# Optimization experiments

Measured on AMD Instinct MI355X. Metric: run time of the kernel, lower is better.

## Reference

```python
import jax, jax.numpy as jnp
import numpy as np

N_NODES = 100000
N_EDGES = 1600000
N_GRAPHS = 256
F_NODE, F_EDGE, HID, OUT = 64, 16, 128, 128
BN_SCALE = 1.0 / np.sqrt(1.0 + 1e-5)  # BatchNorm eval with running mean 0, var 1


def setup_inputs() -> dict:
    key = jax.random.key(0)
    ks = iter(jax.random.split(key, 64))
    inp = {}
    inp["x"] = jax.random.normal(next(ks), (N_NODES, F_NODE), dtype=jnp.float32)
    inp["edge_attr"] = jax.random.normal(next(ks), (N_EDGES, F_EDGE), dtype=jnp.float32)
    inp["edge_index"] = jax.random.randint(next(ks), (2, N_EDGES), 0, N_NODES)
    inp["batch"] = jnp.sort(jax.random.randint(next(ks), (N_NODES,), 0, N_GRAPHS))

    def p(shape, scale):
        return (jax.random.normal(next(ks), shape, dtype=jnp.float32) * scale)

    in_dims = [F_NODE, HID, HID]
    for i, d in enumerate(in_dims):
        inp[f"el_w{i}"] = p((F_EDGE, d), F_EDGE ** -0.5)
        inp[f"el_b{i}"] = jnp.zeros((d,), jnp.float32)
        inp[f"c{i}_w1"] = p((d, HID), d ** -0.5)
        inp[f"c{i}_b1"] = jnp.zeros((HID,), jnp.float32)
        inp[f"c{i}_g"] = jnp.ones((HID,), jnp.float32)
        inp[f"c{i}_bt"] = jnp.zeros((HID,), jnp.float32)
        inp[f"c{i}_w2"] = p((HID, HID), HID ** -0.5)
        inp[f"c{i}_b2"] = jnp.zeros((HID,), jnp.float32)
    inp["o_w1"] = p((HID, OUT), HID ** -0.5)
    inp["o_b1"] = jnp.zeros((OUT,), jnp.float32)
    inp["o_w2"] = p((OUT, OUT), OUT ** -0.5)
    inp["o_b2"] = jnp.zeros((OUT,), jnp.float32)
    return inp


def reference(x, edge_attr,
              el_w0, el_b0, c0_w1, c0_b1, c0_g, c0_bt, c0_w2, c0_b2,
              el_w1, el_b1, c1_w1, c1_b1, c1_g, c1_bt, c1_w2, c1_b2,
              el_w2, el_b2, c2_w1, c2_b1, c2_g, c2_bt, c2_w2, c2_b2,
              o_w1, o_b1, o_w2, o_b2,
              edge_index, batch):
    src, dst = edge_index[0], edge_index[1]
    n = x.shape[0]
    layers = [
        (el_w0, el_b0, c0_w1, c0_b1, c0_g, c0_bt, c0_w2, c0_b2),
        (el_w1, el_b1, c1_w1, c1_b1, c1_g, c1_bt, c1_w2, c1_b2),
        (el_w2, el_b2, c2_w1, c2_b1, c2_g, c2_bt, c2_w2, c2_b2),
    ]
    h = x
    for (ew, eb, w1, b1, g, bt, w2, b2) in layers:
        ea = edge_attr @ ew + eb                              # [E, d]
        msg = jax.nn.relu(h[src] + ea)                        # GINEConv message
        agg = jax.ops.segment_sum(msg, dst, num_segments=n)   # scatter-sum to targets
        hh = h + agg                                          # (1+eps)*x + aggr, eps=0
        hh = hh @ w1 + b1                                     # MLP: Linear
        hh = g * (hh * BN_SCALE) + bt                         # BatchNorm1d (eval)
        hh = jax.nn.relu(hh)
        hh = hh @ w2 + b2                                     # MLP: Linear
        h = jax.nn.relu(hh)                                   # dropout(p=0, eval) + act
    s = jax.ops.segment_sum(h, batch, num_segments=N_GRAPHS)
    cnt = jax.ops.segment_sum(jnp.ones((n,), h.dtype), batch, num_segments=N_GRAPHS)
    pooled = s / jnp.maximum(cnt, 1.0)[:, None]               # scatter-mean pooling
    out = jax.nn.relu(pooled @ o_w1 + o_b1) @ o_w2 + o_b2     # out_lin
    return out
```

## Files before the change

kernel.cpp:

```cpp
#include <hip/hip_runtime.h>
#include <hip/hip_fp16.h>
#include <cstdint>
#include <cstddef>

#define N_NODES_C  100000
#define N_EDGES_C  1600000
#define N_GRAPHS_C 256
#define HID_C      128
#define BN_SCALE_C 0.9999950000374997f

#define SCAN_B 1024
#define SCAN_NB ((N_NODES_C + SCAN_B - 1) / SCAN_B)

typedef _Float16 h2 __attribute__((ext_vector_type(2)));
typedef _Float16 h4 __attribute__((ext_vector_type(4)));
typedef _Float16 h8 __attribute__((ext_vector_type(8)));
typedef float    f4 __attribute__((ext_vector_type(4)));

struct __align__(16) EA8 { h2 p[4]; };
struct __align__(8)  HQ  { h2 a, b; };
struct __align__(16) H8  { __half2 v[4]; };

#if defined(__has_builtin)
#  if __has_builtin(__builtin_amdgcn_fdot2)
#    define HAVE_FDOT2 1
#  endif
#endif
#ifndef HAVE_FDOT2
#  define HAVE_FDOT2 0
#endif

__device__ __forceinline__ float fdot2_(h2 a, h2 b, float c)
{
#if HAVE_FDOT2
    return __builtin_amdgcn_fdot2(a, b, c, false);
#else
    return c + (float)a[0] * (float)b[0] + (float)a[1] * (float)b[1];
#endif
}

__global__ __launch_bounds__(256) void hist_kernel(
    const int* __restrict__ dst, int* __restrict__ counts, int n_edges)
{
    int e = blockIdx.x * 256 + threadIdx.x;
    if (e < n_edges) atomicAdd(&counts[dst[e]], 1);
}

__global__ __launch_bounds__(SCAN_B) void scan1_kernel(
    const int* __restrict__ counts, int* __restrict__ incl,
    int* __restrict__ blocksums, int n)
{
    __shared__ int sdata[SCAN_B];
    const int lid = threadIdx.x;
    const int i = blockIdx.x * SCAN_B + lid;
    sdata[lid] = (i < n) ? counts[i] : 0;
    __syncthreads();
#pragma unroll
    for (int off = 1; off < SCAN_B; off <<= 1) {
        int t = (lid >= off) ? sdata[lid - off] : 0;
        __syncthreads();
        sdata[lid] += t;
        __syncthreads();
    }
    if (i < n) incl[i] = sdata[lid];
    if (lid == SCAN_B - 1) blocksums[blockIdx.x] = sdata[lid];
}

__global__ void scan2_kernel(const int* __restrict__ blocksums,
                             int* __restrict__ blockoffs, int nb)
{
    if (threadIdx.x == 0 && blockIdx.x == 0) {
        int off = 0;
        for (int b = 0; b < nb; ++b) { blockoffs[b] = off; off += blocksums[b]; }
    }
}

__global__ __launch_bounds__(SCAN_B) void scan3_kernel(
    int* __restrict__ incl, const int* __restrict__ blockoffs, int n)
{
    const int i = blockIdx.x * SCAN_B + threadIdx.x;
    if (i < n) incl[i] += blockoffs[blockIdx.x];
}

__global__ __launch_bounds__(256) void initrows_kernel(
    const int* __restrict__ incl, const int* __restrict__ counts,
    int* __restrict__ rowstart, int* __restrict__ cursor, int n)
{
    const int i = blockIdx.x * 256 + threadIdx.x;
    if (i < n) {
        const int rs = incl[i] - counts[i];
        rowstart[i] = rs;
        cursor[i]   = rs;
    }
}

__global__ __launch_bounds__(256) void scatter_ea_kernel(
    const int* __restrict__ src, const int* __restrict__ dst,
    int* __restrict__ cursor, int* __restrict__ perm_src,
    const float* __restrict__ edge_attr, __half* __restrict__ ea_f16,
    int n_edges)
{
    const int e = blockIdx.x * 256 + threadIdx.x;
    if (e >= n_edges) return;

    const float4* p = (const float4*)(edge_attr + (size_t)e * 16);
    const float4 q0 = p[0], q1 = p[1], q2 = p[2], q3 = p[3];

    const int pos = atomicAdd(&cursor[dst[e]], 1);
    perm_src[pos] = src[e];

    H8 a, b;
    a.v[0] = __floats2half2_rn(q0.x, q0.y);
    a.v[1] = __floats2half2_rn(q0.z, q0.w);
    a.v[2] = __floats2half2_rn(q1.x, q1.y);
    a.v[3] = __floats2half2_rn(q1.z, q1.w);
    b.v[0] = __floats2half2_rn(q2.x, q2.y);
    b.v[1] = __floats2half2_rn(q2.z, q2.w);
    b.v[2] = __floats2half2_rn(q3.x, q3.y);
    b.v[3] = __floats2half2_rn(q3.z, q3.w);
    H8* o = (H8*)(ea_f16 + (size_t)pos * 16);
    o[0] = a;
    o[1] = b;
}

__global__ __launch_bounds__(256) void cast_f16_kernel(
    const float* __restrict__ in, _Float16* __restrict__ out, int n4)
{
    const int i = blockIdx.x * 256 + threadIdx.x;
    if (i >= n4) return;
    const float4 v = ((const float4*)in)[i];
    h4 o; o[0] = (_Float16)v.x; o[1] = (_Float16)v.y;
    o[2] = (_Float16)v.z; o[3] = (_Float16)v.w;
    *(h4*)(out + (size_t)i * 4) = o;
}

__global__ __launch_bounds__(256) void transpose_w_kernel(
    const float* __restrict__ w, _Float16* __restrict__ wt, int K, int N)
{
    const int i = blockIdx.x * 256 + threadIdx.x;
    if (i >= K * N) return;
    const int n = i / K;
    const int k = i - n * K;
    wt[(size_t)n * K + k] = (_Float16)w[(size_t)k * N + n];
}

__device__ __forceinline__ float4 eamlp2(const EA8 a0, const EA8 c0,
                                         const h2 (*ew2h)[4], const float4 ebv)
{
    float4 m = {ebv.x, ebv.y, ebv.z, ebv.w};
#pragma unroll
    for (int k = 0; k < 4; ++k) {
        m.x = fdot2_(a0.p[k], ew2h[k][0], m.x);
        m.y = fdot2_(a0.p[k], ew2h[k][1], m.y);
        m.z = fdot2_(a0.p[k], ew2h[k][2], m.z);
        m.w = fdot2_(a0.p[k], ew2h[k][3], m.w);
    }
#pragma unroll
    for (int k = 0; k < 4; ++k) {
        m.x = fdot2_(c0.p[k], ew2h[4 + k][0], m.x);
        m.y = fdot2_(c0.p[k], ew2h[4 + k][1], m.y);
        m.z = fdot2_(c0.p[k], ew2h[4 + k][2], m.z);
        m.w = fdot2_(c0.p[k], ew2h[4 + k][3], m.w);
    }
    return m;
}

template<int DIN>
__global__ __launch_bounds__(256) void gine_agg_kernel(
    const _Float16* __restrict__ hin, const _Float16* __restrict__ ea16,
    const int* __restrict__ perm_src,
    const int* __restrict__ rowstart, const int* __restrict__ rowend,
    const float* __restrict__ ew, const float* __restrict__ eb,
    _Float16* __restrict__ x16, int n_nodes)
{
    constexpr int NQ    = DIN / 4;
    constexpr int SLOTS = 256 / NQ;
    const int fq   = threadIdx.x & (NQ - 1);
    const int slot = threadIdx.x / NQ;
    const int v = blockIdx.x * SLOTS + slot;
    if (v >= n_nodes) return;

    h2 ew2h[8][4];
#pragma unroll
    for (int k2 = 0; k2 < 8; ++k2)
#pragma unroll
        for (int fi = 0; fi < 4; ++fi) {
            h2 t;
            t[0] = (_Float16)ew[(size_t)(2 * k2)     * DIN + fq * 4 + fi];
            t[1] = (_Float16)ew[(size_t)(2 * k2 + 1) * DIN + fq * 4 + fi];
            ew2h[k2][fi] = t;
        }
    const float4 ebv = *(const float4*)(eb + fq * 4);

    const int s0 = rowstart[v];
    const int s1 = rowend[v];

    float4 acc = {0.f, 0.f, 0.f, 0.f};
    int j = s0;

    for (; j + 4 <= s1; j += 4) {
        const int sn0 = perm_src[j + 0];
        const int sn1 = perm_src[j + 1];
        const int sn2 = perm_src[j + 2];
        const int sn3 = perm_src[j + 3];
        const EA8* pe = (const EA8*)(ea16 + (size_t)j * 16);
        const EA8 a0 = pe[0], c0 = pe[1], a1 = pe[2], c1 = pe[3];
        const EA8 a2 = pe[4], c2 = pe[5], a3 = pe[6], c3 = pe[7];
        const HQ hq0 = *(const HQ*)(hin + (size_t)sn0 * DIN + fq * 4);
        const HQ hq1 = *(const HQ*)(hin + (size_t)sn1 * DIN + fq * 4);
        const HQ hq2 = *(const HQ*)(hin + (size_t)sn2 * DIN + fq * 4);
        const HQ hq3 = *(const HQ*)(hin + (size_t)sn3 * DIN + fq * 4);

        const float4 m0 = eamlp2(a0, c0, ew2h, ebv);
        const float4 m1 = eamlp2(a1, c1, ew2h, ebv);
        const float4 m2 = eamlp2(a2, c2, ew2h, ebv);
        const float4 m3 = eamlp2(a3, c3, ew2h, ebv);

        acc.x += fmaxf(m0.x + (float)hq0.a[0], 0.f) + fmaxf(m1.x + (float)hq1.a[0], 0.f)
               + fmaxf(m2.x + (float)hq2.a[0], 0.f) + fmaxf(m3.x + (float)hq3.a[0], 0.f);
        acc.y += fmaxf(m0.y + (float)hq0.a[1], 0.f) + fmaxf(m1.y + (float)hq1.a[1], 0.f)
               + fmaxf(m2.y + (float)hq2.a[1], 0.f) + fmaxf(m3.y + (float)hq3.a[1], 0.f);
        acc.z += fmaxf(m0.z + (float)hq0.b[0], 0.f) + fmaxf(m1.z + (float)hq1.b[0], 0.f)
               + fmaxf(m2.z + (float)hq2.b[0], 0.f) + fmaxf(m3.z + (float)hq3.b[0], 0.f);
        acc.w += fmaxf(m0.w + (float)hq0.b[1], 0.f) + fmaxf(m1.w + (float)hq1.b[1], 0.f)
               + fmaxf(m2.w + (float)hq2.b[1], 0.f) + fmaxf(m3.w + (float)hq3.b[1], 0.f);
    }
    if (j + 2 <= s1) {
        const int sn0 = perm_src[j + 0];
        const int sn1 = perm_src[j + 1];
        const EA8* pe = (const EA8*)(ea16 + (size_t)j * 16);
        const EA8 a0 = pe[0], c0 = pe[1], a1 = pe[2], c1 = pe[3];
        const HQ hq0 = *(const HQ*)(hin + (size_t)sn0 * DIN + fq * 4);
        const HQ hq1 = *(const HQ*)(hin + (size_t)sn1 * DIN + fq * 4);
        const float4 m0 = eamlp2(a0, c0, ew2h, ebv);
        const float4 m1 = eamlp2(a1, c1, ew2h, ebv);
        acc.x += fmaxf(m0.x + (float)hq0.a[0], 0.f) + fmaxf(m1.x + (float)hq1.a[0], 0.f);
        acc.y += fmaxf(m0.y + (float)hq0.a[1], 0.f) + fmaxf(m1.y + (float)hq1.a[1], 0.f);
        acc.z += fmaxf(m0.z + (float)hq0.b[0], 0.f) + fmaxf(m1.z + (float)hq1.b[0], 0.f);
        acc.w += fmaxf(m0.w + (float)hq0.b[1], 0.f) + fmaxf(m1.w + (float)hq1.b[1], 0.f);
        j += 2;
    }
    if (j < s1) {
        const int sn = perm_src[j];
        const EA8* pe = (const EA8*)(ea16 + (size_t)j * 16);
        const EA8 a0 = pe[0], c0 = pe[1];
        const HQ hq = *(const HQ*)(hin + (size_t)sn * DIN + fq * 4);
        const float4 m0 = eamlp2(a0, c0, ew2h, ebv);
        acc.x += fmaxf(m0.x + (float)hq.a[0], 0.f);
        acc.y += fmaxf(m0.y + (float)hq.a[1], 0.f);
        acc.z += fmaxf(m0.z + (float)hq.b[0], 0.f);
        acc.w += fmaxf(m0.w + (float)hq.b[1], 0.f);
    }

    const HQ hv = *(const HQ*)(hin + (size_t)v * DIN + fq * 4);
    h4 o;
    o[0] = (_Float16)(acc.x + (float)hv.a[0]);
    o[1] = (_Float16)(acc.y + (float)hv.a[1]);
    o[2] = (_Float16)(acc.z + (float)hv.b[0]);
    o[3] = (_Float16)(acc.w + (float)hv.b[1]);
    *(h4*)(x16 + (size_t)v * DIN + fq * 4) = o;
}

template<int DIN>
__global__ __launch_bounds__(64) void node_mfma_kernel(
    const _Float16* __restrict__ x16,
    const _Float16* __restrict__ w1t, const float* __restrict__ b1,
    const float* __restrict__ gm, const float* __restrict__ bt,
    const _Float16* __restrict__ w2t, const float* __restrict__ b2,
    _Float16* __restrict__ h16out, int n_tiles)
{
    constexpr int STP = HID_C + 8;
    __shared__ _Float16 s_t[16][STP];

    const int lane = threadIdx.x;
    const int tile = blockIdx.x;
    const int node0 = tile * 16;
    const int ln   = lane & 15;
    const int quad = lane >> 4;

    constexpr int NKS = DIN / 32;
    h8 af[NKS];
#pragma unroll
    for (int ks = 0; ks < NKS; ++ks)
        af[ks] = *(const h8*)(x16 + (size_t)(node0 + ln) * DIN + ks * 32 + quad * 8);

#pragma unroll
    for (int nt = 0; nt < 8; ++nt) {
        const int col = nt * 16 + ln;
        const float bv = b1[col];
        f4 acc = {bv, bv, bv, bv};
#pragma unroll
        for (int ks = 0; ks < NKS; ++ks) {
            const h8 bf = *(const h8*)(w1t + (size_t)col * DIN + ks * 32 + quad * 8);
            acc = __builtin_amdgcn_mfma_f32_16x16x32_f16(af[ks], bf, acc, 0, 0, 0);
        }
        const float gv = gm[col], btv = bt[col];
#pragma unroll
        for (int r = 0; r < 4; ++r) {
            const float t = fmaxf(fmaf(acc[r] * BN_SCALE_C, gv, btv), 0.f);
            s_t[quad * 4 + r][col] = (_Float16)t;
        }
    }
    __syncthreads();

    h8 af2[4];
#pragma unroll
    for (int ks = 0; ks < 4; ++ks)
        af2[ks] = *(const h8*)&s_t[ln][ks * 32 + quad * 8];

#pragma unroll
    for (int nt = 0; nt < 8; ++nt) {
        const int col = nt * 16 + ln;
        const float bv = b2[col];
        f4 acc = {bv, bv, bv, bv};
#pragma unroll
        for (int ks = 0; ks < 4; ++ks) {
            const h8 bf = *(const h8*)(w2t + (size_t)col * HID_C + ks * 32 + quad * 8);
            acc = __builtin_amdgcn_mfma_f32_16x16x32_f16(af2[ks], bf, acc, 0, 0, 0);
        }
#pragma unroll
        for (int r = 0; r < 4; ++r) {
            const int node = node0 + quad * 4 + r;
            h16out[(size_t)node * HID_C + col] = (_Float16)fmaxf(acc[r], 0.f);
        }
    }
}

__global__ __launch_bounds__(256) void pool_kernel(
    const _Float16* __restrict__ hfin, const int* __restrict__ batch,
    const float* __restrict__ w1, const float* __restrict__ b1,
    const float* __restrict__ w2, const float* __restrict__ b2,
    float* __restrict__ out, int n_nodes)
{
    const int gid = blockIdx.x;

    int lo = 0, hi = n_nodes;
    while (lo < hi) { int mid = (lo + hi) >> 1; if (batch[mid] < gid) lo = mid + 1; else hi = mid; }
    const int start = lo;
    hi = n_nodes;
    while (lo < hi) { int mid = (lo + hi) >> 1; if (batch[mid] < gid + 1) lo = mid + 1; else hi = mid; }
    const int end = lo;

    const int f = threadIdx.x & (HID_C - 1);
    const int half = threadIdx.x >> 7;

    float sum = 0.f;
    for (int n = start + half; n < end; n += 2)
        sum += (float)hfin[(size_t)n * HID_C + f];

    __shared__ float s_sum[2][HID_C];
    __shared__ float s_p[HID_C];
    __shared__ float s_t[HID_C];
    s_sum[half][f] = sum;
    __syncthreads();

    if (threadIdx.x < HID_C) {
        const float cnt = (float)(end - start);
        s_p[f] = (s_sum[0][f] + s_sum[1][f]) / fmaxf(cnt, 1.f);
    }
    __syncthreads();

    if (threadIdx.x < HID_C) {
        float acc = b1[f];
        for (int k = 0; k < HID_C; ++k) acc = fmaf(s_p[k], w1[k * HID_C + f], acc);
        s_t[f] = fmaxf(acc, 0.f);
    }
    __syncthreads();

    if (threadIdx.x < HID_C) {
        float acc = b2[f];
        for (int k = 0; k < HID_C; ++k) acc = fmaf(s_t[k], w2[k * HID_C + f], acc);
        out[(size_t)gid * HID_C + f] = acc;
    }
}

extern "C" void kernel_launch(void* const* d_in, const int* in_sizes, int n_in,
                              void* d_out, int out_size, void* d_ws, size_t ws_size,
                              hipStream_t stream)
{
    const float* x         = (const float*)d_in[0];
    const float* edge_attr = (const float*)d_in[1];
    const int*   edge_index= (const int*)  d_in[2];
    const int*   batch     = (const int*)  d_in[3];
    const int*   src = edge_index;
    const int*   dst = edge_index + N_EDGES_C;

    const float* el_w[3] = {(const float*)d_in[4],  (const float*)d_in[12], (const float*)d_in[20]};
    const float* el_b[3] = {(const float*)d_in[5],  (const float*)d_in[13], (const float*)d_in[21]};
    const float* c_w1[3] = {(const float*)d_in[6],  (const float*)d_in[14], (const float*)d_in[22]};
    const float* c_b1[3] = {(const float*)d_in[7],  (const float*)d_in[15], (const float*)d_in[23]};
    const float* c_g [3] = {(const float*)d_in[8],  (const float*)d_in[16], (const float*)d_in[24]};
    const float* c_bt[3] = {(const float*)d_in[9],  (const float*)d_in[17], (const float*)d_in[25]};
    const float* c_w2[3] = {(const float*)d_in[10], (const float*)d_in[18], (const float*)d_in[26]};
    const float* c_b2[3] = {(const float*)d_in[11], (const float*)d_in[19], (const float*)d_in[27]};
    const float* o_w1 = (const float*)d_in[28];
    const float* o_b1 = (const float*)d_in[29];
    const float* o_w2 = (const float*)d_in[30];
    const float* o_b2 = (const float*)d_in[31];

    char* wsp = (char*)d_ws;
    size_t used = 0;
    auto alloc = [&](size_t bytes) { char* p = wsp + used; used += (bytes + 255) & ~(size_t)255; return p; };
    int*   counts   = (int*)alloc((size_t)N_NODES_C * 4);
    int*   incl     = (int*)alloc((size_t)N_NODES_C * 4);
    int*   rowstart = (int*)alloc((size_t)N_NODES_C * 4);
    int*   cursor   = (int*)alloc((size_t)N_NODES_C * 4);
    int*   blocksums= (int*)alloc(128 * 4);
    int*   blockoffs= (int*)alloc(128 * 4);
    int*   perm_src = (int*)alloc((size_t)N_EDGES_C * 4);
    _Float16* ea_f16 = (_Float16*)alloc((size_t)N_EDGES_C * 16 * 2);
    _Float16* x16    = (_Float16*)alloc((size_t)N_NODES_C * HID_C * 2);
    _Float16* h16_a  = (_Float16*)alloc((size_t)N_NODES_C * HID_C * 2);
    _Float16* h16_b  = (_Float16*)alloc((size_t)N_NODES_C * HID_C * 2);
    _Float16* x_f16  = (_Float16*)alloc((size_t)N_NODES_C * 64 * 2);
    _Float16* w1t[3], *w2t[3];
    for (int l = 0; l < 3; ++l) {
        w1t[l] = (_Float16*)alloc((size_t)HID_C * HID_C * 2);
        w2t[l] = (_Float16*)alloc((size_t)HID_C * HID_C * 2);
    }
    (void)ws_size;

    hipMemsetAsync(counts, 0, (size_t)N_NODES_C * 4, stream);
    hist_kernel<<<(N_EDGES_C + 255) / 256, 256, 0, stream>>>(dst, counts, N_EDGES_C);
    scan1_kernel<<<SCAN_NB, SCAN_B, 0, stream>>>(counts, incl, blocksums, N_NODES_C);
    scan2_kernel<<<1, 64, 0, stream>>>(blocksums, blockoffs, SCAN_NB);
    scan3_kernel<<<SCAN_NB, SCAN_B, 0, stream>>>(incl, blockoffs, N_NODES_C);
    initrows_kernel<<<(N_NODES_C + 255) / 256, 256, 0, stream>>>(incl, counts, rowstart,
                                                                 cursor, N_NODES_C);
    scatter_ea_kernel<<<(N_EDGES_C + 255) / 256, 256, 0, stream>>>(
        src, dst, cursor, perm_src, edge_attr, (__half*)ea_f16, N_EDGES_C);
    cast_f16_kernel<<<(N_NODES_C * 64 / 4 + 255) / 256, 256, 0, stream>>>(
        x, x_f16, N_NODES_C * 64 / 4);
    for (int l = 0; l < 3; ++l) {
        const int K1 = (l == 0) ? 64 : HID_C;
        transpose_w_kernel<<<(K1 * HID_C + 255) / 256, 256, 0, stream>>>(
            c_w1[l], w1t[l], K1, HID_C);
        transpose_w_kernel<<<(HID_C * HID_C + 255) / 256, 256, 0, stream>>>(
            c_w2[l], w2t[l], HID_C, HID_C);
    }

    const int n_tiles = N_NODES_C / 16;

    gine_agg_kernel<64><<<(N_NODES_C + 15) / 16, 256, 0, stream>>>(
        x_f16, ea_f16, perm_src, rowstart, incl, el_w[0], el_b[0],
        x16, N_NODES_C);
    node_mfma_kernel<64><<<n_tiles, 64, 0, stream>>>(
        x16, w1t[0], c_b1[0], c_g[0], c_bt[0], w2t[0], c_b2[0],
        h16_a, n_tiles);
    gine_agg_kernel<128><<<(N_NODES_C + 7) / 8, 256, 0, stream>>>(
        h16_a, ea_f16, perm_src, rowstart, incl, el_w[1], el_b[1],
        x16, N_NODES_C);
    node_mfma_kernel<128><<<n_tiles, 64, 0, stream>>>(
        x16, w1t[1], c_b1[1], c_g[1], c_bt[1], w2t[1], c_b2[1],
        h16_b, n_tiles);
    gine_agg_kernel<128><<<(N_NODES_C + 7) / 8, 256, 0, stream>>>(
        h16_b, ea_f16, perm_src, rowstart, incl, el_w[2], el_b[2],
        x16, N_NODES_C);
    node_mfma_kernel<128><<<n_tiles, 64, 0, stream>>>(
        x16, w1t[2], c_b1[2], c_g[2], c_bt[2], w2t[2], c_b2[2],
        h16_a, n_tiles);

    pool_kernel<<<N_GRAPHS_C, 256, 0, stream>>>(h16_a, batch, o_w1, o_b1, o_w2, o_b2,
                                                (float*)d_out, N_NODES_C);
}
```

Baseline: 936.4 us.

## Compute GINE edge linear with MFMA, one wave per destination node

Replaces the per-thread fdot2 edge-attribute projection with a 16x16x32 f16 MFMA per 16-edge tile. Each wavefront now owns one destination node at a time and strides over nodes with a fixed grid of 2048 blocks. The aim is to move the edge-linear arithmetic, which previously took most of the ALU work in the aggregation, onto the matrix cores. In exchange, half of each MFMA's K dimension is zero padding, edge tiles are padded when a node's degree is not a multiple of 16, and the source-feature gathers become scalar fp16 loads instead of vector loads.

```diff
diff --git a/kernel.cpp b/kernel.cpp
--- a/kernel.cpp
+++ b/kernel.cpp
@@ -12,32 +12,15 @@
 #define SCAN_B 1024
 #define SCAN_NB ((N_NODES_C + SCAN_B - 1) / SCAN_B)
 
+#define AGG_BLOCKS 2048
+#define AGG_WAVES  (AGG_BLOCKS * 4)
+
 typedef _Float16 h2 __attribute__((ext_vector_type(2)));
 typedef _Float16 h4 __attribute__((ext_vector_type(4)));
 typedef _Float16 h8 __attribute__((ext_vector_type(8)));
 typedef float    f4 __attribute__((ext_vector_type(4)));
 
-struct __align__(16) EA8 { h2 p[4]; };
-struct __align__(8)  HQ  { h2 a, b; };
 struct __align__(16) H8  { __half2 v[4]; };
-
-#if defined(__has_builtin)
-#  if __has_builtin(__builtin_amdgcn_fdot2)
-#    define HAVE_FDOT2 1
-#  endif
-#endif
-#ifndef HAVE_FDOT2
-#  define HAVE_FDOT2 0
-#endif
-
-__device__ __forceinline__ float fdot2_(h2 a, h2 b, float c)
-{
-#if HAVE_FDOT2
-    return __builtin_amdgcn_fdot2(a, b, c, false);
-#else
-    return c + (float)a[0] * (float)b[0] + (float)a[1] * (float)b[1];
-#endif
-}
 
 __global__ __launch_bounds__(256) void hist_kernel(
     const int* __restrict__ dst, int* __restrict__ counts, int n_edges)
@@ -144,121 +127,92 @@
     wt[(size_t)n * K + k] = (_Float16)w[(size_t)k * N + n];
 }
 
-__device__ __forceinline__ float4 eamlp2(const EA8 a0, const EA8 c0,
-                                         const h2 (*ew2h)[4], const float4 ebv)
-{
-    float4 m = {ebv.x, ebv.y, ebv.z, ebv.w};
-#pragma unroll
-    for (int k = 0; k < 4; ++k) {
-        m.x = fdot2_(a0.p[k], ew2h[k][0], m.x);
-        m.y = fdot2_(a0.p[k], ew2h[k][1], m.y);
-        m.z = fdot2_(a0.p[k], ew2h[k][2], m.z);
-        m.w = fdot2_(a0.p[k], ew2h[k][3], m.w);
-    }
-#pragma unroll
-    for (int k = 0; k < 4; ++k) {
-        m.x = fdot2_(c0.p[k], ew2h[4 + k][0], m.x);
-        m.y = fdot2_(c0.p[k], ew2h[4 + k][1], m.y);
-        m.z = fdot2_(c0.p[k], ew2h[4 + k][2], m.z);
-        m.w = fdot2_(c0.p[k], ew2h[4 + k][3], m.w);
-    }
-    return m;
-}
-
 template<int DIN>
-__global__ __launch_bounds__(256) void gine_agg_kernel(
+__global__ __launch_bounds__(256) void gine_agg_mfma_kernel(
     const _Float16* __restrict__ hin, const _Float16* __restrict__ ea16,
     const int* __restrict__ perm_src,
     const int* __restrict__ rowstart, const int* __restrict__ rowend,
     const float* __restrict__ ew, const float* __restrict__ eb,
     _Float16* __restrict__ x16, int n_nodes)
 {
-    constexpr int NQ    = DIN / 4;
-    constexpr int SLOTS = 256 / NQ;
-    const int fq   = threadIdx.x & (NQ - 1);
-    const int slot = threadIdx.x / NQ;
-    const int v = blockIdx.x * SLOTS + slot;
-    if (v >= n_nodes) return;
-
-    h2 ew2h[8][4];
-#pragma unroll
-    for (int k2 = 0; k2 < 8; ++k2)
-#pragma unroll
-        for (int fi = 0; fi < 4; ++fi) {
-            h2 t;
-            t[0] = (_Float16)ew[(size_t)(2 * k2)     * DIN + fq * 4 + fi];
-            t[1] = (_Float16)ew[(size_t)(2 * k2 + 1) * DIN + fq * 4 + fi];
-            ew2h[k2][fi] = t;
-        }
-    const float4 ebv = *(const float4*)(eb + fq * 4);
-
-    const int s0 = rowstart[v];
-    const int s1 = rowend[v];
-
-    float4 acc = {0.f, 0.f, 0.f, 0.f};
-    int j = s0;
-
-    for (; j + 4 <= s1; j += 4) {
-        const int sn0 = perm_src[j + 0];
-        const int sn1 = perm_src[j + 1];
-        const int sn2 = perm_src[j + 2];
-        const int sn3 = perm_src[j + 3];
-        const EA8* pe = (const EA8*)(ea16 + (size_t)j * 16);
-        const EA8 a0 = pe[0], c0 = pe[1], a1 = pe[2], c1 = pe[3];
-        const EA8 a2 = pe[4], c2 = pe[5], a3 = pe[6], c3 = pe[7];
-        const HQ hq0 = *(const HQ*)(hin + (size_t)sn0 * DIN + fq * 4);
-        const HQ hq1 = *(const HQ*)(hin + (size_t)sn1 * DIN + fq * 4);
-        const HQ hq2 = *(const HQ*)(hin + (size_t)sn2 * DIN + fq * 4);
-        const HQ hq3 = *(const HQ*)(hin + (size_t)sn3 * DIN + fq * 4);
-
-        const float4 m0 = eamlp2(a0, c0, ew2h, ebv);
-        const float4 m1 = eamlp2(a1, c1, ew2h, ebv);
-        const float4 m2 = eamlp2(a2, c2, ew2h, ebv);
-        const float4 m3 = eamlp2(a3, c3, ew2h, ebv);
-
-        acc.x += fmaxf(m0.x + (float)hq0.a[0], 0.f) + fmaxf(m1.x + (float)hq1.a[0], 0.f)
-               + fmaxf(m2.x + (float)hq2.a[0], 0.f) + fmaxf(m3.x + (float)hq3.a[0], 0.f);
-        acc.y += fmaxf(m0.y + (float)hq0.a[1], 0.f) + fmaxf(m1.y + (float)hq1.a[1], 0.f)
-               + fmaxf(m2.y + (float)hq2.a[1], 0.f) + fmaxf(m3.y + (float)hq3.a[1], 0.f);
-        acc.z += fmaxf(m0.z + (float)hq0.b[0], 0.f) + fmaxf(m1.z + (float)hq1.b[0], 0.f)
-               + fmaxf(m2.z + (float)hq2.b[0], 0.f) + fmaxf(m3.z + (float)hq3.b[0], 0.f);
-        acc.w += fmaxf(m0.w + (float)hq0.b[1], 0.f) + fmaxf(m1.w + (float)hq1.b[1], 0.f)
-               + fmaxf(m2.w + (float)hq2.b[1], 0.f) + fmaxf(m3.w + (float)hq3.b[1], 0.f);
-    }
-    if (j + 2 <= s1) {
-        const int sn0 = perm_src[j + 0];
-        const int sn1 = perm_src[j + 1];
-        const EA8* pe = (const EA8*)(ea16 + (size_t)j * 16);
-        const EA8 a0 = pe[0], c0 = pe[1], a1 = pe[2], c1 = pe[3];
-        const HQ hq0 = *(const HQ*)(hin + (size_t)sn0 * DIN + fq * 4);
-        const HQ hq1 = *(const HQ*)(hin + (size_t)sn1 * DIN + fq * 4);
-        const float4 m0 = eamlp2(a0, c0, ew2h, ebv);
-        const float4 m1 = eamlp2(a1, c1, ew2h, ebv);
-        acc.x += fmaxf(m0.x + (float)hq0.a[0], 0.f) + fmaxf(m1.x + (float)hq1.a[0], 0.f);
-        acc.y += fmaxf(m0.y + (float)hq0.a[1], 0.f) + fmaxf(m1.y + (float)hq1.a[1], 0.f);
-        acc.z += fmaxf(m0.z + (float)hq0.b[0], 0.f) + fmaxf(m1.z + (float)hq1.b[0], 0.f);
-        acc.w += fmaxf(m0.w + (float)hq0.b[1], 0.f) + fmaxf(m1.w + (float)hq1.b[1], 0.f);
-        j += 2;
-    }
-    if (j < s1) {
-        const int sn = perm_src[j];
-        const EA8* pe = (const EA8*)(ea16 + (size_t)j * 16);
-        const EA8 a0 = pe[0], c0 = pe[1];
-        const HQ hq = *(const HQ*)(hin + (size_t)sn * DIN + fq * 4);
-        const float4 m0 = eamlp2(a0, c0, ew2h, ebv);
-        acc.x += fmaxf(m0.x + (float)hq.a[0], 0.f);
-        acc.y += fmaxf(m0.y + (float)hq.a[1], 0.f);
-        acc.z += fmaxf(m0.z + (float)hq.b[0], 0.f);
-        acc.w += fmaxf(m0.w + (float)hq.b[1], 0.f);
-    }
-
-    const HQ hv = *(const HQ*)(hin + (size_t)v * DIN + fq * 4);
-    h4 o;
-    o[0] = (_Float16)(acc.x + (float)hv.a[0]);
-    o[1] = (_Float16)(acc.y + (float)hv.a[1]);
-    o[2] = (_Float16)(acc.z + (float)hv.b[0]);
-    o[3] = (_Float16)(acc.w + (float)hv.b[1]);
-    *(h4*)(x16 + (size_t)v * DIN + fq * 4) = o;
+    constexpr int NB  = DIN / 16;
+    constexpr int NB4 = NB / 4;
+
+    const int lane = threadIdx.x & 63;
+    const int wid  = blockIdx.x * 4 + (threadIdx.x >> 6);
+    const int ln   = lane & 15;
+    const int quad = lane >> 4;
+
+    h8 bfrag[NB];
+    float ebf[NB];
+#pragma unroll
+    for (int b = 0; b < NB; ++b) {
+        const int f = b * 16 + ln;
+        h8 t = {};
+        if (quad < 2) {
+#pragma unroll
+            for (int j = 0; j < 8; ++j)
+                t[j] = (_Float16)ew[(size_t)(quad * 8 + j) * DIN + f];
+        }
+        bfrag[b] = t;
+        ebf[b] = eb[f];
+    }
+    const h8 zero8 = {};
+
+    for (int v = wid; v < n_nodes; v += AGG_WAVES) {
+        const int s0 = rowstart[v];
+        const int s1 = rowend[v];
+        const int deg = s1 - s0;
+
+        float acc[NB];
+#pragma unroll
+        for (int b = 0; b < NB; ++b) acc[b] = 0.f;
+
+        for (int t0 = 0; t0 < deg; t0 += 16) {
+            h8 af = zero8;
+            if (quad < 2) {
+                int eA = s0 + t0 + ln;
+                if (eA >= s1) eA = s1 - 1;
+                af = *(const h8*)(ea16 + (size_t)eA * 16 + quad * 8);
+            }
+            int srcs[4];
+#pragma unroll
+            for (int r = 0; r < 4; ++r) {
+                int er = s0 + t0 + quad * 4 + r;
+                if (er >= s1) er = s1 - 1;
+                srcs[r] = perm_src[er];
+            }
+
+#pragma unroll
+            for (int b = 0; b < NB; ++b) {
+                f4 c = {ebf[b], ebf[b], ebf[b], ebf[b]};
+                c = __builtin_amdgcn_mfma_f32_16x16x32_f16(af, bfrag[b], c, 0, 0, 0);
+                const int f = b * 16 + ln;
+                float s = 0.f;
+#pragma unroll
+                for (int r = 0; r < 4; ++r) {
+                    const float hv = (float)hin[(size_t)srcs[r] * DIN + f];
+                    const float t = fmaxf(c[r] + hv, 0.f);
+                    s += ((t0 + quad * 4 + r) < deg) ? t : 0.f;
+                }
+                acc[b] += s;
+            }
+        }
+
+#pragma unroll
+        for (int b = 0; b < NB; ++b) {
+            acc[b] += __shfl_xor(acc[b], 16);
+            acc[b] += __shfl_xor(acc[b], 32);
+        }
+
+#pragma unroll
+        for (int bb = 0; bb < NB4; ++bb) {
+            const int b = quad * NB4 + bb;
+            const int f = b * 16 + ln;
+            const float hv = (float)hin[(size_t)v * DIN + f];
+            x16[(size_t)v * DIN + f] = (_Float16)(acc[b] + hv);
+        }
+    }
 }
 
 template<int DIN>
@@ -441,19 +395,19 @@
 
     const int n_tiles = N_NODES_C / 16;
 
-    gine_agg_kernel<64><<<(N_NODES_C + 15) / 16, 256, 0, stream>>>(
+    gine_agg_mfma_kernel<64><<<AGG_BLOCKS, 256, 0, stream>>>(
         x_f16, ea_f16, perm_src, rowstart, incl, el_w[0], el_b[0],
         x16, N_NODES_C);
     node_mfma_kernel<64><<<n_tiles, 64, 0, stream>>>(
         x16, w1t[0], c_b1[0], c_g[0], c_bt[0], w2t[0], c_b2[0],
         h16_a, n_tiles);
-    gine_agg_kernel<128><<<(N_NODES_C + 7) / 8, 256, 0, stream>>>(
+    gine_agg_mfma_kernel<128><<<AGG_BLOCKS, 256, 0, stream>>>(
         h16_a, ea_f16, perm_src, rowstart, incl, el_w[1], el_b[1],
         x16, N_NODES_C);
     node_mfma_kernel<128><<<n_tiles, 64, 0, stream>>>(
         x16, w1t[1], c_b1[1], c_g[1], c_bt[1], w2t[1], c_b2[1],
         h16_b, n_tiles);
-    gine_agg_kernel<128><<<(N_NODES_C + 7) / 8, 256, 0, stream>>>(
+    gine_agg_mfma_kernel<128><<<AGG_BLOCKS, 256, 0, stream>>>(
         h16_b, ea_f16, perm_src, rowstart, incl, el_w[2], el_b[2],
         x16, N_NODES_C);
     node_mfma_kernel<128><<<n_tiles, 64, 0, stream>>>(
```

After: 1.329 ms. 41.9% more time.
